# Kernel tuning notes

Measured on AMD Instinct MI355X. Metric: run time of the kernel, lower is better.

## Reference

```python
import jax, jax.numpy as jnp
import numpy as np

KS = 3
PAD = 1
N = KS * KS  # 9 sampling points


def setup_inputs() -> dict:
    key = jax.random.key(0)
    k1, k2, k3 = jax.random.split(key, 3)
    B, C, H, W = 8, 64, 96, 96
    OUT = 64
    x = jax.random.normal(k1, (B, C, H, W), jnp.float32)
    offset = jax.random.normal(k2, (B, 2 * N, H, W), jnp.float32)
    conv_w = jax.random.normal(k3, (OUT, C * N, KS, KS), jnp.float32) * 0.02
    conv_b = jnp.zeros((OUT,), jnp.float32)
    return {"x": x, "offset": offset, "conv_w": conv_w, "conv_b": conv_b}


def _deform_gather(x, offset):
    # zero-pad spatially (nn.ZeroPad2d)
    xp = jnp.pad(x, ((0, 0), (0, 0), (PAD, PAD), (PAD, PAD)))
    b, c, h, w = xp.shape
    _, _, ho, wo = offset.shape
    # base kernel grid (row, col) pairs, shape (N, 2)
    grid = jnp.stack(
        jnp.meshgrid(jnp.arange(KS), jnp.arange(KS), indexing='ij'), axis=-1
    ).reshape(-1, 2).astype(offset.dtype)
    # offsets: (b, 2N, ho, wo) -> (b, ho, wo, N, 2)
    off = offset.transpose(0, 2, 3, 1).reshape(b, ho, wo, N, 2)
    p = grid[None, None, None] + off                       # (b, ho, wo, N, 2)
    # replicate torch's non-contiguous permute+reshape exactly (row-major)
    p = p.transpose(0, 3, 1, 2, 4).reshape(b, 2 * N, ho, wo)
    qx = jnp.clip(p[:, :N], 0, w - 1)                      # (b, N, ho, wo)
    qy = jnp.clip(p[:, N:], 0, h - 1)
    x0 = jnp.clip(jnp.floor(qx).astype(jnp.int32), 0, w - 1)
    x1 = jnp.clip(x0 + 1, 0, w - 1)
    y0 = jnp.clip(jnp.floor(qy).astype(jnp.int32), 0, h - 1)
    y1 = jnp.clip(y0 + 1, 0, h - 1)
    xf = xp.reshape(b, c, h * w)

    def g(iy, ix):
        idx = (iy * w + ix).reshape(b, 1, -1)              # (b, 1, N*ho*wo)
        v = jnp.take_along_axis(
            xf, jnp.broadcast_to(idx, (b, c, idx.shape[-1])), axis=2)
        return v.reshape(b, c, N, ho, wo)

    v00 = g(y0, x0); v01 = g(y0, x1); v10 = g(y1, x0); v11 = g(y1, x1)
    wx = (qx - x0.astype(qx.dtype))[:, None]               # (b, 1, N, ho, wo)
    wy = (qy - y0.astype(qy.dtype))[:, None]
    val = (v00 * (1 - wx) + v01 * wx) * (1 - wy) + (v10 * (1 - wx) + v11 * wx) * wy
    # (b, c, N, ho, wo) -> (b, c, ho, wo, N) -> (b, c*N, ho, wo)
    return val.transpose(0, 1, 3, 4, 2).reshape(b, c * N, ho, wo)


def reference(x, offset, conv_w, conv_b):
    xo = _deform_gather(x, offset)
    out = jax.lax.conv_general_dilated(
        xo, conv_w, window_strides=(1, 1), padding='VALID',
        dimension_numbers=('NCHW', 'OIHW', 'NCHW'))
    return out + conv_b[None, :, None, None]
```

## Files before the change

### kernel.cpp

```cpp
#include <hip/hip_runtime.h>

typedef short bf16x8 __attribute__((ext_vector_type(8)));
typedef float f32x4  __attribute__((ext_vector_type(4)));

#define Sx 9216
#define ROWW 96
#define WB_USHORTS 331776
#define OW 94
#define XO_USHORTS ((size_t)8 * 96 * ROWW * 576)
#define XT_OFF_BYTES (2 * (size_t)WB_USHORTS + 2 * XO_USHORTS)
#define NEED_NEW (XT_OFF_BYTES + (size_t)8 * Sx * 64 * 4)

__device__ __forceinline__ unsigned short bf16r(float f) {
    unsigned int u = __float_as_uint(f);
    u += 0x7fffu + ((u >> 16) & 1u);
    return (unsigned short)(u >> 16);
}

__device__ __forceinline__ void gload16(const void* g, void* l) {
    __builtin_amdgcn_global_load_lds(
        (const __attribute__((address_space(1))) void*)g,
        (__attribute__((address_space(3))) void*)l, 16, 0, 0);
}

__global__ __launch_bounds__(256)
void wprep_k(const float* __restrict__ w, unsigned short* __restrict__ Wb) {
    int id = blockIdx.x * 256 + threadIdx.x;
    if (id >= 162 * 4 * 64) return;
    int lane = id & 63;
    int fm   = id >> 6;
    int mt   = fm & 3;
    int step = fm >> 2;
    int qc   = step / 18;
    int rs   = step - qc * 18;
    int t    = rs >> 1;
    int q32  = rs & 1;
    int o    = mt * 16 + (lane & 15);
    int cib  = q32 * 32 + (lane >> 4) * 8;
    unsigned short v[8];
    #pragma unroll
    for (int j = 0; j < 8; ++j) {
        int qorig = (cib + j) * 9 + qc;
        v[j] = bf16r(w[(size_t)o * 5184 + qorig * 9 + t]);
    }
    uint4 u;
    u.x = v[0] | ((unsigned)v[1] << 16);
    u.y = v[2] | ((unsigned)v[3] << 16);
    u.z = v[4] | ((unsigned)v[5] << 16);
    u.w = v[6] | ((unsigned)v[7] << 16);
    *(uint4*)(Wb + (size_t)id * 8) = u;
}

__global__ __launch_bounds__(256)
void xt_k(const float* __restrict__ x, float* __restrict__ xt) {
    __shared__ float t[64][65];
    const int tid = threadIdx.x;
    const int r2b = blockIdx.x * 64;
    const int b   = blockIdx.y;
    const int qq  = tid >> 6;
    const int ll  = tid & 63;
    #pragma unroll
    for (int cc = 0; cc < 16; ++cc) {
        int ci = cc * 4 + qq;
        t[ci][ll] = x[((size_t)(b * 64 + ci)) * Sx + r2b + ll];
    }
    __syncthreads();
    #pragma unroll
    for (int rr = 0; rr < 16; ++rr) {
        int r2l = rr * 4 + qq;
        xt[((size_t)b * Sx + r2b + r2l) * 64 + ll] = t[ll][r2l];
    }
}

__device__ __forceinline__ void decode_phase1(
        const float* __restrict__ ob, int x0b, int y,
        int (*sA)[288], float (*sW)[288], int tid) {
    for (int e = tid; e < 288; e += 256) {
        int chr = e >> 5;
        int xl  = e & 31;
        int r2  = y * 96 + x0b + xl;
        int n   = r2 % 9;
        int r   = chr * 1024 + r2 / 9;
        float q2[2];
        #pragma unroll
        for (int c2 = 0; c2 < 2; ++c2) {
            int k    = n + 9 * c2;
            int f    = k * Sx + r;
            int nn   = f / 18432;
            int t    = f - nn * 18432;
            int comp = t & 1;
            int pos  = t >> 1;
            int nd3  = nn / 3;
            float gg = comp ? (float)(nn - nd3 * 3) : (float)nd3;
            q2[c2] = gg + ob[(size_t)(2 * nn + comp) * Sx + pos];
        }
        float qx = fminf(fmaxf(q2[0], 0.f), 97.f);
        float qy = fminf(fmaxf(q2[1], 0.f), 97.f);
        int x0 = (int)qx; if (x0 > 97) x0 = 97;
        int y0 = (int)qy; if (y0 > 97) y0 = 97;
        float fx = qx - (float)x0;
        float fy = qy - (float)y0;
        int x1 = x0 + 1; if (x1 > 97) x1 = 97;
        int y1 = y0 + 1; if (y1 > 97) y1 = 97;
        int ix0 = x0 - 1, ix1 = x1 - 1, iy0 = y0 - 1, iy1 = y1 - 1;
        float vx0 = (ix0 >= 0 && ix0 < 96) ? 1.f : 0.f;
        float vx1 = (ix1 >= 0 && ix1 < 96) ? 1.f : 0.f;
        float vy0 = (iy0 >= 0 && iy0 < 96) ? 1.f : 0.f;
        float vy1 = (iy1 >= 0 && iy1 < 96) ? 1.f : 0.f;
        int cx0 = min(max(ix0, 0), 95), cx1 = min(max(ix1, 0), 95);
        int cy0 = min(max(iy0, 0), 95), cy1 = min(max(iy1, 0), 95);
        sW[0][e] = (1.f - fx) * (1.f - fy) * vx0 * vy0;
        sW[1][e] = fx * (1.f - fy) * vx1 * vy0;
        sW[2][e] = (1.f - fx) * fy * vx0 * vy1;
        sW[3][e] = fx * fy * vx1 * vy1;
        sA[0][e] = cy0 * 96 + cx0;
        sA[1][e] = cy0 * 96 + cx1;
        sA[2][e] = cy1 * 96 + cx0;
        sA[3][e] = cy1 * 96 + cx1;
    }
}

__global__ __launch_bounds__(256, 4)
void gather_xt(const float* __restrict__ xt, const float* __restrict__ off,
               unsigned short* __restrict__ xo) {
    __shared__ int   sA[4][288];
    __shared__ float sW[4][288];
    const int tid = threadIdx.x;
    const int x0b = blockIdx.x * 32;
    const int y   = blockIdx.y;
    const int b   = blockIdx.z;
    decode_phase1(off + (size_t)b * 18 * Sx, x0b, y, sA, sW, tid);
    __syncthreads();

    const int lane = tid & 63;
    const int wv   = tid >> 6;
    const float* xtb = xt + (size_t)b * Sx * 64 + lane;
    unsigned short* xob =
        xo + ((size_t)(b * 96 + y) * ROWW + x0b) * 576 + lane;

    #pragma unroll 4
    for (int i = 0; i < 72; ++i) {
        int e   = wv * 72 + i;
        int chr = e >> 5;
        int xl  = e & 31;
        float v = sW[0][e] * xtb[(size_t)sA[0][e] * 64]
                + sW[1][e] * xtb[(size_t)sA[1][e] * 64]
                + sW[2][e] * xtb[(size_t)sA[2][e] * 64]
                + sW[3][e] * xtb[(size_t)sA[3][e] * 64];
        xob[xl * 576 + chr * 64] = bf16r(v);
    }
}

__global__ __launch_bounds__(256, 2)
void gather_fb(const float* __restrict__ x, const float* __restrict__ off,
               unsigned short* __restrict__ xo) {
    __shared__ int   sA[4][288];
    __shared__ float sW[4][288];
    const int tid = threadIdx.x;
    const int x0b = blockIdx.x * 32;
    const int y   = blockIdx.y;
    const int b   = blockIdx.z;
    decode_phase1(off + (size_t)b * 18 * Sx, x0b, y, sA, sW, tid);
    __syncthreads();

    const int xl = tid & 31;
    const int g  = tid >> 5;
    const float* xb = x + (size_t)b * 64 * Sx + (size_t)g * 8 * Sx;
    uint4* dst = (uint4*)(xo + ((size_t)(b * 96 + y) * ROWW + (x0b + xl)) * 576) + g;

    #pragma unroll
    for (int chr = 0; chr < 9; ++chr) {
        int e = chr * 32 + xl;
        int   a00 = sA[0][e], a01 = sA[1][e], a10 = sA[2][e], a11 = sA[3][e];
        float w00 = sW[0][e], w01 = sW[1][e], w10 = sW[2][e], w11 = sW[3][e];
        unsigned short v[8];
        #pragma unroll
        for (int i = 0; i < 8; ++i) {
            const float* xc = xb + (size_t)i * Sx;
            v[i] = bf16r(w00 * xc[a00] + w01 * xc[a01]
                       + w10 * xc[a10] + w11 * xc[a11]);
        }
        uint4 u;
        u.x = v[0] | ((unsigned)v[1] << 16);
        u.y = v[2] | ((unsigned)v[3] << 16);
        u.z = v[4] | ((unsigned)v[5] << 16);
        u.w = v[6] | ((unsigned)v[7] << 16);
        dst[chr * 8] = u;
    }
}

__global__ __launch_bounds__(192, 3)
void conv_mfma(const unsigned short* __restrict__ xo,
               const unsigned short* __restrict__ Wb,
               const float* __restrict__ bias,
               float* __restrict__ out) {
    const int lane = threadIdx.x & 63;
    const int wn   = threadIdx.x >> 6;
    const int lin  = blockIdx.x;
    const int b    = lin & 7;
    const int rest = lin >> 3;
    const int mh   = rest & 1;
    const int p    = rest >> 1;

    __shared__ unsigned short tile[4 * 6144 + 256];
    char* tb = (char*)tile;

    f32x4 acc[2][2][2];
    #pragma unroll
    for (int m = 0; m < 2; ++m)
        #pragma unroll
        for (int ro = 0; ro < 2; ++ro)
            #pragma unroll
            for (int xf = 0; xf < 2; ++xf)
                acc[m][ro][xf] = (f32x4){0.f, 0.f, 0.f, 0.f};

    const bf16x8* W8 = (const bf16x8*)Wb;

    const int xl  = lane >> 3;
    const int sl  = lane & 7;
    const int swz = (sl ^ xl) * 8;
    const size_t rowbase = (size_t)(b * 96 + 2 * p) * (ROWW * 576);

    for (int qc = 0; qc < 9; ++qc) {
        if (qc) __syncthreads();
        #pragma unroll
        for (int i = 0; i < 16; ++i) {
            int j   = wn * 16 + i;
            int row = j / 12;
            int xi  = j - row * 12;
            const unsigned short* src =
                xo + rowbase + (size_t)row * (ROWW * 576)
                   + (size_t)(xi * 8 + xl) * 576 + qc * 64 + swz;
            gload16(src, tile + row * 6144 + xi * 512);
        }
        asm volatile("s_waitcnt vmcnt(0)" ::: "memory");
        __syncthreads();

        #pragma unroll
        for (int st = 0; st < 18; ++st) {
            const int t = st >> 1, q32 = st & 1;
            const int ky = t / 3, kx = t - (t / 3) * 3;
            const int step = qc * 18 + st;
            bf16x8 a0 = W8[(step * 4 + mh * 2 + 0) * 64 + lane];
            bf16x8 a1 = W8[(step * 4 + mh * 2 + 1) * 64 + lane];
            bf16x8 bf[2][2];
            #pragma unroll
            for (int ro = 0; ro < 2; ++ro) {
                #pragma unroll
                for (int xf = 0; xf < 2; ++xf) {
                    int xpix = wn * 32 + xf * 16 + (lane & 15) + kx;
                    int slot = (q32 * 4 + (lane >> 4)) ^ (xpix & 7);
                    bf[ro][xf] = *(const bf16x8*)(tb + (ro + ky) * 12288
                                                    + xpix * 128 + slot * 16);
                }
            }
            __builtin_amdgcn_s_setprio(1);
            #pragma unroll
            for (int ro = 0; ro < 2; ++ro) {
                #pragma unroll
                for (int xf = 0; xf < 2; ++xf) {
                    acc[0][ro][xf] = __builtin_amdgcn_mfma_f32_16x16x32_bf16(a0, bf[ro][xf], acc[0][ro][xf], 0, 0, 0);
                    acc[1][ro][xf] = __builtin_amdgcn_mfma_f32_16x16x32_bf16(a1, bf[ro][xf], acc[1][ro][xf], 0, 0, 0);
                }
            }
            __builtin_amdgcn_s_setprio(0);
        }
    }

    #pragma unroll
    for (int m = 0; m < 2; ++m) {
        #pragma unroll
        for (int ro = 0; ro < 2; ++ro) {
            #pragma unroll
            for (int xf = 0; xf < 2; ++xf) {
                int ox = wn * 32 + xf * 16 + (lane & 15);
                if (ox < OW) {
                    int oyr = 2 * p + ro;
                    #pragma unroll
                    for (int j = 0; j < 4; ++j) {
                        int o = mh * 32 + m * 16 + (lane >> 4) * 4 + j;
                        out[(((size_t)b * 64 + o) * OW + oyr) * OW + ox] =
                            acc[m][ro][xf][j] + bias[o];
                    }
                }
            }
        }
    }
}

extern "C" void kernel_launch(void* const* d_in, const int* in_sizes, int n_in,
                              void* d_out, int out_size, void* d_ws, size_t ws_size,
                              hipStream_t stream) {
    const float* x    = (const float*)d_in[0];
    const float* off  = (const float*)d_in[1];
    const float* w    = (const float*)d_in[2];
    const float* bias = (const float*)d_in[3];
    unsigned short* ws16 = (unsigned short*)d_ws;
    unsigned short* Wb   = ws16;
    unsigned short* xo   = ws16 + WB_USHORTS;

    wprep_k<<<162, 256, 0, stream>>>(w, Wb);
    if (ws_size >= NEED_NEW) {
        float* xt = (float*)((char*)d_ws + XT_OFF_BYTES);
        xt_k<<<dim3(144, 8), 256, 0, stream>>>(x, xt);
        gather_xt<<<dim3(3, 96, 8), 256, 0, stream>>>(xt, off, xo);
    } else {
        gather_fb<<<dim3(3, 96, 8), 256, 0, stream>>>(x, off, xo);
    }
    conv_mfma<<<752, 192, 0, stream>>>(xo, Wb, bias, (float*)d_out);
}
```

Baseline: 123.7 us.

## Use 32x32 MFMA conv with split-K over channel groups and reduction pass

Adds a new convolution kernel that uses 32x32x16 bf16 MFMA instructions, with each block covering all 64 output channels and splitting the 9 channel chunks into two halves (5 and 4) across blocks. The second half writes partial sums to a scratch buffer, which a separate reduce kernel adds into the output. The weights are re-laid out to match the 32x32 fragment format. The aim is higher MFMA efficiency and fewer redundant tile loads, at the cost of an extra partial-sum write and read plus an extra kernel launch.

```diff
diff --git a/kernel.cpp b/kernel.cpp
--- a/kernel.cpp
+++ b/kernel.cpp
@@ -2,6 +2,7 @@
 
 typedef short bf16x8 __attribute__((ext_vector_type(8)));
 typedef float f32x4  __attribute__((ext_vector_type(4)));
+typedef float f32x16 __attribute__((ext_vector_type(16)));
 
 #define Sx 9216
 #define ROWW 96
@@ -10,6 +11,7 @@
 #define XO_USHORTS ((size_t)8 * 96 * ROWW * 576)
 #define XT_OFF_BYTES (2 * (size_t)WB_USHORTS + 2 * XO_USHORTS)
 #define NEED_NEW (XT_OFF_BYTES + (size_t)8 * Sx * 64 * 4)
+#define NOUT 4524032
 
 __device__ __forceinline__ unsigned short bf16r(float f) {
     unsigned int u = __float_as_uint(f);
@@ -21,6 +23,32 @@
     __builtin_amdgcn_global_load_lds(
         (const __attribute__((address_space(1))) void*)g,
         (__attribute__((address_space(3))) void*)l, 16, 0, 0);
+}
+
+__global__ __launch_bounds__(256)
+void wprep32_k(const float* __restrict__ w, unsigned short* __restrict__ Wb) {
+    int id = blockIdx.x * 256 + threadIdx.x;
+    if (id >= 648 * 64) return;
+    int lane = id & 63;
+    int fm   = id >> 6;
+    int m    = fm & 1;
+    int rest = fm >> 1;
+    int k16  = rest & 3;
+    int rest2= rest >> 2;
+    int qc   = rest2 / 9;
+    int t    = rest2 - qc * 9;
+    int o    = m * 32 + (lane & 31);
+    int cb   = k16 * 16 + (lane >> 5) * 8;
+    unsigned short v[8];
+    #pragma unroll
+    for (int j = 0; j < 8; ++j)
+        v[j] = bf16r(w[(size_t)o * 5184 + ((cb + j) * 9 + qc) * 9 + t]);
+    uint4 u;
+    u.x = v[0] | ((unsigned)v[1] << 16);
+    u.y = v[2] | ((unsigned)v[3] << 16);
+    u.z = v[4] | ((unsigned)v[5] << 16);
+    u.w = v[6] | ((unsigned)v[7] << 16);
+    *(uint4*)(Wb + (size_t)id * 8) = u;
 }
 
 __global__ __launch_bounds__(256)
@@ -189,11 +217,113 @@
     }
 }
 
+__global__ __launch_bounds__(192, 2)
+void conv32_k(const unsigned short* __restrict__ xo,
+              const unsigned short* __restrict__ Wb,
+              const float* __restrict__ bias,
+              float* __restrict__ out, float* __restrict__ pbuf) {
+    const int lane = threadIdx.x & 63;
+    const int wn   = threadIdx.x >> 6;
+    const int lin  = blockIdx.x;
+    const int b    = lin & 7;
+    const int rest = lin >> 3;
+    const int ks   = rest & 1;
+    const int p    = rest >> 1;
+
+    __shared__ unsigned short tile[4 * 6656];
+    const char* tb = (const char*)tile;
+
+    f32x16 acc[2][2];
+    #pragma unroll
+    for (int m = 0; m < 2; ++m)
+        #pragma unroll
+        for (int ro = 0; ro < 2; ++ro)
+            acc[m][ro] = (f32x16){0.f,0.f,0.f,0.f,0.f,0.f,0.f,0.f,
+                                  0.f,0.f,0.f,0.f,0.f,0.f,0.f,0.f};
+
+    const bf16x8* W8 = (const bf16x8*)Wb;
+    const int xl  = lane >> 3;
+    const int sl  = lane & 7;
+    const int swz = (sl ^ xl) * 8;
+    const size_t rowbase = (size_t)(b * 96 + 2 * p) * (ROWW * 576);
+
+    const int qc0 = ks ? 5 : 0;
+    const int qc1 = ks ? 9 : 5;
+
+    for (int qc = qc0; qc < qc1; ++qc) {
+        if (qc > qc0) __syncthreads();
+        #pragma unroll
+        for (int i = 0; i < 18; ++i) {
+            int idx = wn + 3 * i;
+            if (idx < 52) {
+                int row = idx / 13;
+                int xi  = idx - row * 13;
+                gload16(xo + rowbase + (size_t)row * (ROWW * 576)
+                           + (size_t)(xi * 8 + xl) * 576 + qc * 64 + swz,
+                        tile + row * 6656 + xi * 512);
+            }
+        }
+        asm volatile("s_waitcnt vmcnt(0)" ::: "memory");
+        __syncthreads();
+
+        #pragma unroll
+        for (int st = 0; st < 36; ++st) {
+            const int t = st >> 2, k16 = st & 3;
+            const int ky = t / 3, kx = t - (t / 3) * 3;
+            const int fb2 = ((qc * 9 + t) * 4 + k16) * 2;
+            bf16x8 a0 = W8[(fb2 + 0) * 64 + lane];
+            bf16x8 a1 = W8[(fb2 + 1) * 64 + lane];
+            const int xpix = wn * 32 + (lane & 31) + kx;
+            const int slot = (k16 * 2 + (lane >> 5)) ^ (xpix & 7);
+            bf16x8 b0 = *(const bf16x8*)(tb + (0 + ky) * 13312 + xpix * 128 + slot * 16);
+            bf16x8 b1 = *(const bf16x8*)(tb + (1 + ky) * 13312 + xpix * 128 + slot * 16);
+            __builtin_amdgcn_s_setprio(1);
+            acc[0][0] = __builtin_amdgcn_mfma_f32_32x32x16_bf16(a0, b0, acc[0][0], 0, 0, 0);
+            acc[0][1] = __builtin_amdgcn_mfma_f32_32x32x16_bf16(a0, b1, acc[0][1], 0, 0, 0);
+            acc[1][0] = __builtin_amdgcn_mfma_f32_32x32x16_bf16(a1, b0, acc[1][0], 0, 0, 0);
+            acc[1][1] = __builtin_amdgcn_mfma_f32_32x32x16_bf16(a1, b1, acc[1][1], 0, 0, 0);
+            __builtin_amdgcn_s_setprio(0);
+        }
+    }
+
+    const int ox = wn * 32 + (lane & 31);
+    float* dst = ks ? pbuf : out;
+    if (ox < OW) {
+        #pragma unroll
+        for (int m = 0; m < 2; ++m) {
+            #pragma unroll
+            for (int ro = 0; ro < 2; ++ro) {
+                const int oyr = 2 * p + ro;
+                #pragma unroll
+                for (int reg = 0; reg < 16; ++reg) {
+                    int row = (reg & 3) + 8 * (reg >> 2) + 4 * (lane >> 5);
+                    int o = m * 32 + row;
+                    float v = acc[m][ro][reg];
+                    if (!ks) v += bias[o];
+                    dst[(((size_t)b * 64 + o) * OW + oyr) * OW + ox] = v;
+                }
+            }
+        }
+    }
+}
+
+__global__ __launch_bounds__(256)
+void reduce_k(float* __restrict__ out, const float* __restrict__ pbuf) {
+    const size_t N4 = NOUT / 4;
+    for (size_t i = blockIdx.x * 256 + threadIdx.x; i < N4;
+         i += (size_t)gridDim.x * 256) {
+        float4 a = ((const float4*)out)[i];
+        float4 c = ((const float4*)pbuf)[i];
+        a.x += c.x; a.y += c.y; a.z += c.z; a.w += c.w;
+        ((float4*)out)[i] = a;
+    }
+}
+
 __global__ __launch_bounds__(192, 3)
-void conv_mfma(const unsigned short* __restrict__ xo,
-               const unsigned short* __restrict__ Wb,
-               const float* __restrict__ bias,
-               float* __restrict__ out) {
+void conv_fb(const unsigned short* __restrict__ xo,
+             const unsigned short* __restrict__ Wb,
+             const float* __restrict__ bias,
+             float* __restrict__ out) {
     const int lane = threadIdx.x & 63;
     const int wn   = threadIdx.x >> 6;
     const int lin  = blockIdx.x;
@@ -215,7 +345,6 @@
                 acc[m][ro][xf] = (f32x4){0.f, 0.f, 0.f, 0.f};
 
     const bf16x8* W8 = (const bf16x8*)Wb;
-
     const int xl  = lane >> 3;
     const int sl  = lane & 7;
     const int swz = (sl ^ xl) * 8;
@@ -228,10 +357,9 @@
             int j   = wn * 16 + i;
             int row = j / 12;
             int xi  = j - row * 12;
-            const unsigned short* src =
-                xo + rowbase + (size_t)row * (ROWW * 576)
-                   + (size_t)(xi * 8 + xl) * 576 + qc * 64 + swz;
-            gload16(src, tile + row * 6144 + xi * 512);
+            gload16(xo + rowbase + (size_t)row * (ROWW * 576)
+                       + (size_t)(xi * 8 + xl) * 576 + qc * 64 + swz,
+                    tile + row * 6144 + xi * 512);
         }
         asm volatile("s_waitcnt vmcnt(0)" ::: "memory");
         __syncthreads();
@@ -254,7 +382,6 @@
                                                     + xpix * 128 + slot * 16);
                 }
             }
-            __builtin_amdgcn_s_setprio(1);
             #pragma unroll
             for (int ro = 0; ro < 2; ++ro) {
                 #pragma unroll
@@ -263,7 +390,6 @@
                     acc[1][ro][xf] = __builtin_amdgcn_mfma_f32_16x16x32_bf16(a1, bf[ro][xf], acc[1][ro][xf], 0, 0, 0);
                 }
             }
-            __builtin_amdgcn_s_setprio(0);
         }
     }
 
@@ -299,13 +425,17 @@
     unsigned short* Wb   = ws16;
     unsigned short* xo   = ws16 + WB_USHORTS;
 
-    wprep_k<<<162, 256, 0, stream>>>(w, Wb);
     if (ws_size >= NEED_NEW) {
         float* xt = (float*)((char*)d_ws + XT_OFF_BYTES);
+        wprep32_k<<<162, 256, 0, stream>>>(w, Wb);
         xt_k<<<dim3(144, 8), 256, 0, stream>>>(x, xt);
         gather_xt<<<dim3(3, 96, 8), 256, 0, stream>>>(xt, off, xo);
+        float* pbuf = xt;
+        conv32_k<<<752, 192, 0, stream>>>(xo, Wb, bias, (float*)d_out, pbuf);
+        reduce_k<<<2048, 256, 0, stream>>>((float*)d_out, pbuf);
     } else {
+        wprep_k<<<162, 256, 0, stream>>>(w, Wb);
         gather_fb<<<dim3(3, 96, 8), 256, 0, stream>>>(x, off, xo);
-    }
-    conv_mfma<<<752, 192, 0, stream>>>(xo, Wb, bias, (float*)d_out);
-}
+        conv_fb<<<752, 192, 0, stream>>>(xo, Wb, bias, (float*)d_out);
+    }
+}
```

Result: slower. 143.9 us (+16.4%).
